# Optimization experiments

Measured on AMD Instinct MI355X. Metric: run time of the kernel, lower is better.

## Reference

```python
import jax, jax.numpy as jnp
import numpy as np

B, S, D = 4, 2048, 1024
H = 16
HD = D // H

def setup_inputs() -> dict:
    key = jax.random.key(0)
    ks = jax.random.split(key, 6)
    scale = 0.02
    return {
        "x": jax.random.normal(ks[0], (B, S, D), dtype=jnp.float32),
        "W_q": jax.random.normal(ks[1], (D, D), dtype=jnp.float32) * scale,
        "W_k": jax.random.normal(ks[2], (D, D), dtype=jnp.float32) * scale,
        "W_v": jax.random.normal(ks[3], (D, D), dtype=jnp.float32) * scale,
        "W_o": jax.random.normal(ks[4], (D, D), dtype=jnp.float32) * scale,
        "b_o": jax.random.normal(ks[5], (D,), dtype=jnp.float32) * scale,
    }

def reference(x, W_q, W_k, W_v, W_o, b_o):
    b, s, d = x.shape
    # projections, split heads: [b, h, s, hd]
    q = (x @ W_q).reshape(b, s, H, HD).transpose(0, 2, 1, 3)
    k = (x @ W_k).reshape(b, s, H, HD).transpose(0, 2, 1, 3)
    v = (x @ W_v).reshape(b, s, H, HD).transpose(0, 2, 1, 3)
    scores = jnp.einsum('bhqd,bhkd->bhqk', q, k)
    causal = jnp.triu(jnp.ones((s, s), dtype=bool), k=1)
    scores = jnp.where(causal, -jnp.inf, scores)
    # module divides by sqrt(hd) after masking; -inf stays -inf
    attn = jax.nn.softmax(scores / jnp.sqrt(jnp.float32(HD)), axis=-1)
    ctx = jnp.einsum('bhqk,bhkd->bhqd', attn, v)
    ctx = ctx.transpose(0, 2, 1, 3).reshape(b, s, d)
    return ctx @ W_o + b_o
```

## Files before the change

kernel.cpp:

```cpp
#include <hip/hip_runtime.h>
#include <hip/hip_bf16.h>
#include <math.h>

typedef __attribute__((ext_vector_type(8))) short bf16x8;
typedef __attribute__((ext_vector_type(4))) float f32x4;
typedef unsigned short u16;
typedef __hip_bfloat16 HB;

#define B_ 4
#define S_ 2048
#define D_ 1024
#define H_ 16
#define HD_ 64

__device__ __forceinline__ u16 f2b(float f) {
  HB h = __float2bfloat16(f);
  return *reinterpret_cast<u16*>(&h);
}
__device__ __forceinline__ void store1(HB* p, float v) { *p = __float2bfloat16(v); }
__device__ __forceinline__ void store1(float* p, float v) { *p = v; }

__device__ __forceinline__ float fexp2(float x) {
#if __has_builtin(__builtin_amdgcn_exp2f)
  return __builtin_amdgcn_exp2f(x);
#else
  return exp2f(x);
#endif
}

__device__ __forceinline__ void glds16(const u16* g, u16* l) {
  __builtin_amdgcn_global_load_lds(
      (const __attribute__((address_space(1))) void*)g,
      (__attribute__((address_space(3))) void*)l, 16, 0, 0);
}

__global__ __launch_bounds__(256) void cast_x(const float* __restrict__ xin,
                                              u16* __restrict__ xout) {
  const long i0 = ((long)blockIdx.x * 256 + threadIdx.x) * 8;
  bf16x8 r;
#pragma unroll
  for (int j = 0; j < 8; ++j) r[j] = (short)f2b(xin[i0 + j]);
  *(bf16x8*)(xout + i0) = r;
}

__global__ __launch_bounds__(256) void transpose_w(
    const float* __restrict__ w0, const float* __restrict__ w1,
    const float* __restrict__ w2, const float* __restrict__ w3,
    u16* __restrict__ out) {
  __shared__ __align__(16) u16 T[64 * 72];
  const float* Ws[4] = {w0, w1, w2, w3};
  const float* W = Ws[blockIdx.z];
  u16* Wt = out + (long)blockIdx.z * (1 << 20);
  const int t = threadIdx.x;
  const int r = t >> 3;
  const int c8 = (t & 7) * 8;
#pragma unroll
  for (int it = 0; it < 2; ++it) {
    const int row = blockIdx.y * 64 + it * 32 + r;
    const float* src = W + (long)row * D_ + blockIdx.x * 64 + c8;
#pragma unroll
    for (int j = 0; j < 8; ++j) T[(c8 + j) * 72 + it * 32 + r] = f2b(src[j]);
  }
  __syncthreads();
#pragma unroll
  for (int it = 0; it < 2; ++it) {
    const int row = it * 32 + r;
    bf16x8 v = *(const bf16x8*)(&T[row * 72 + c8]);
    *(bf16x8*)(Wt + (long)(blockIdx.x * 64 + row) * D_ + blockIdx.y * 64 + c8) = v;
  }
}

template <typename OT>
__global__ __launch_bounds__(256) void gemm_bt128(
    const u16* __restrict__ A, const u16* __restrict__ BTb, long bt_stride,
    OT* __restrict__ Cb, long c_stride, const float* __restrict__ bias,
    u16* __restrict__ vt, int scale_q, int M, int N, int K) {
  const u16* BT = BTb + (long)blockIdx.z * bt_stride;
  OT* C = Cb + (long)blockIdx.z * c_stride;

  __shared__ __align__(16) u16 As[128 * 32];
  __shared__ __align__(16) u16 Bs[128 * 32];

  const int tid = threadIdx.x;
  const int w = tid >> 6, lane = tid & 63;
  const int qr = lane & 15, quad = lane >> 4;
  const int wm = w >> 1, wn = w & 1;

  const long rowA0 = (long)blockIdx.y * 128;
  const long rowB0 = (long)blockIdx.x * 128;

  const int sr = lane >> 2;
  const int sc8 = ((lane & 3) ^ ((lane >> 3) & 3)) * 8;
  const long arow = rowA0 + w * 16 + sr;
  const long brow = rowB0 + w * 16 + sr;
  u16* asd0 = As + (w * 16) * 32;
  u16* asd1 = As + (64 + w * 16) * 32;
  u16* bsd0 = Bs + (w * 16) * 32;
  u16* bsd1 = Bs + (64 + w * 16) * 32;

  f32x4 acc[4][4] = {};

  for (int k0 = 0; k0 < K; k0 += 32) {
    __syncthreads();
    glds16(A + arow * K + k0 + sc8, asd0);
    glds16(A + (arow + 64) * K + k0 + sc8, asd1);
    glds16(BT + brow * K + k0 + sc8, bsd0);
    glds16(BT + (brow + 64) * K + k0 + sc8, bsd1);
    __syncthreads();

    bf16x8 af[4], bf[4];
#pragma unroll
    for (int ms = 0; ms < 4; ++ms) {
      const int m = wm * 64 + ms * 16 + qr;
      af[ms] = *(const bf16x8*)(&As[m * 32 + ((quad ^ ((m >> 1) & 3)) * 8)]);
    }
#pragma unroll
    for (int ns = 0; ns < 4; ++ns) {
      const int n = wn * 64 + ns * 16 + qr;
      bf[ns] = *(const bf16x8*)(&Bs[n * 32 + ((quad ^ ((n >> 1) & 3)) * 8)]);
    }

#pragma unroll
    for (int ms = 0; ms < 4; ++ms)
#pragma unroll
      for (int ns = 0; ns < 4; ++ns)
        acc[ms][ns] = __builtin_amdgcn_mfma_f32_16x16x32_bf16(
            af[ms], bf[ns], acc[ms][ns], 0, 0, 0);
  }

  if (vt && blockIdx.z == 2) {
#pragma unroll
    for (int ns = 0; ns < 4; ++ns) {
      const int col = (int)rowB0 + wn * 64 + ns * 16 + qr;
#pragma unroll
      for (int ms = 0; ms < 4; ++ms) {
        const long row = rowA0 + wm * 64 + ms * 16 + quad * 4;
        const long b = row >> 11, s = row & 2047;
        ushort4 pk;
        pk.x = f2b(acc[ms][ns][0]); pk.y = f2b(acc[ms][ns][1]);
        pk.z = f2b(acc[ms][ns][2]); pk.w = f2b(acc[ms][ns][3]);
        *(ushort4*)(vt + ((b * H_ + (col >> 6)) * HD_ + (col & 63)) * S_ + s) = pk;
      }
    }
    return;
  }

  const float qs = (scale_q && blockIdx.z == 0) ? 0.18033688011112042f : 1.f;
#pragma unroll
  for (int ns = 0; ns < 4; ++ns) {
    const long col = rowB0 + wn * 64 + ns * 16 + qr;
    const float bv = bias ? bias[col] : 0.f;
#pragma unroll
    for (int ms = 0; ms < 4; ++ms) {
      const long row = rowA0 + wm * 64 + ms * 16 + quad * 4;
#pragma unroll
      for (int r = 0; r < 4; ++r)
        store1(&C[(row + r) * (long)N + col], acc[ms][ns][r] * qs + bv);
    }
  }
}

__global__ __launch_bounds__(256) void attn5(
    const u16* __restrict__ Q, const u16* __restrict__ Kg,
    const u16* __restrict__ Vt, u16* __restrict__ ctx) {
  __shared__ __align__(16) u16 KV[2][2][64 * 64];
  __shared__ __align__(16) u16 Pl[4][16 * 64];

  const int tid = threadIdx.x;
  const int w = tid >> 6, lane = tid & 63;
  const int qr = lane & 15, quad = lane >> 4;
  const int bh = blockIdx.x;
  const int b = bh >> 4, h = bh & 15;

  const long baseQK = ((long)b * S_) * D_ + h * HD_;
  const long baseVt = (long)bh * HD_ * S_;

  const int sr8 = lane >> 3;
  const int sc8 = ((lane & 7) ^ sr8) * 8;

  const int tiles2[2] = {(int)blockIdx.y, 15 - (int)blockIdx.y};

#pragma unroll
  for (int ti = 0; ti < 2; ++ti) {
    const int q0 = tiles2[ti] * 128;
    const int qbase = q0 + w * 32;

    bf16x8 aq[2][2];
#pragma unroll
    for (int i = 0; i < 2; ++i) {
      const u16* qp_ = Q + baseQK + (long)(qbase + i * 16 + qr) * D_;
      aq[i][0] = *(const bf16x8*)(qp_ + quad * 8);
      aq[i][1] = *(const bf16x8*)(qp_ + 32 + quad * 8);
    }

    float li[2] = {};
    f32x4 o[2][4] = {};

    const int nkt = q0 / 64 + 2;

#pragma unroll
    for (int t = 0; t < 2; ++t) {
      const int r = t * 32 + w * 8 + sr8;
      glds16(Kg + baseQK + (long)r * D_ + sc8, &KV[0][0][(t * 32 + w * 8) * 64]);
      glds16(Vt + baseVt + (long)r * S_ + sc8, &KV[0][1][(t * 32 + w * 8) * 64]);
    }

    for (int kt = 0; kt < nkt; ++kt) {
      const int kbase = kt * 64;
      const int buf = kt & 1;

      __syncthreads();

      if (kt + 1 < nkt) {
        const int nb = kbase + 64;
#pragma unroll
        for (int t = 0; t < 2; ++t) {
          const int r = t * 32 + w * 8 + sr8;
          glds16(Kg + baseQK + (long)(nb + r) * D_ + sc8,
                 &KV[buf ^ 1][0][(t * 32 + w * 8) * 64]);
          glds16(Vt + baseVt + (long)r * S_ + nb + sc8,
                 &KV[buf ^ 1][1][(t * 32 + w * 8) * 64]);
        }
      }

      const u16* Ksb = KV[buf][0];
      const u16* Vsb = KV[buf][1];

      bf16x8 kf[4][2];
#pragma unroll
      for (int ns = 0; ns < 4; ++ns) {
        const int row = ns * 16 + qr;
        kf[ns][0] = *(const bf16x8*)(&Ksb[row * 64 + ((quad ^ (row & 7)) * 8)]);
        kf[ns][1] =
            *(const bf16x8*)(&Ksb[row * 64 + (((4 + quad) ^ (row & 7)) * 8)]);
      }

      f32x4 s[2][4] = {};
#pragma unroll
      for (int i = 0; i < 2; ++i)
#pragma unroll
        for (int ns = 0; ns < 4; ++ns) {
          s[i][ns] = __builtin_amdgcn_mfma_f32_16x16x32_bf16(
              kf[ns][0], aq[i][0], s[i][ns], 0, 0, 0);
          s[i][ns] = __builtin_amdgcn_mfma_f32_16x16x32_bf16(
              kf[ns][1], aq[i][1], s[i][ns], 0, 0, 0);
        }

#pragma unroll
      for (int i = 0; i < 2; ++i) {
        if (kbase + 64 > qbase + i * 16) {
          const int qrow = qbase + i * 16 + qr;
#pragma unroll
          for (int ns = 0; ns < 4; ++ns) {
            const int kc = kbase + ns * 16 + quad * 4;
#pragma unroll
            for (int r = 0; r < 4; ++r)
              if (kc + r > qrow) s[i][ns][r] = -1.0e30f;
          }
        }
      }

      bf16x8 vf[4][2];
#pragma unroll
      for (int ns = 0; ns < 4; ++ns) {
        const int row = ns * 16 + qr;
        vf[ns][0] = *(const bf16x8*)(&Vsb[row * 64 + ((quad ^ (row & 7)) * 8)]);
        vf[ns][1] =
            *(const bf16x8*)(&Vsb[row * 64 + (((4 + quad) ^ (row & 7)) * 8)]);
      }

#pragma unroll
      for (int i = 0; i < 2; ++i) {
        float ps = 0.f;
#pragma unroll
        for (int ns = 0; ns < 4; ++ns) {
          const float p0 = fexp2(s[i][ns][0]);
          const float p1 = fexp2(s[i][ns][1]);
          const float p2 = fexp2(s[i][ns][2]);
          const float p3 = fexp2(s[i][ns][3]);
          ps += (p0 + p1) + (p2 + p3);
          ushort4 pk;
          pk.x = f2b(p0); pk.y = f2b(p1); pk.z = f2b(p2); pk.w = f2b(p3);
          *(ushort4*)(&Pl[w][qr * 64 +
                             (((2 * ns + (quad >> 1)) ^ (qr & 7)) * 8) +
                             (quad & 1) * 4]) = pk;
        }
        ps += __shfl_xor(ps, 16, 64);
        ps += __shfl_xor(ps, 32, 64);
        li[i] += ps;

        bf16x8 pf0 = *(const bf16x8*)(&Pl[w][qr * 64 + ((quad ^ (qr & 7)) * 8)]);
        bf16x8 pf1 =
            *(const bf16x8*)(&Pl[w][qr * 64 + (((4 + quad) ^ (qr & 7)) * 8)]);
#pragma unroll
        for (int ns = 0; ns < 4; ++ns) {
          o[i][ns] = __builtin_amdgcn_mfma_f32_16x16x32_bf16(pf0, vf[ns][0],
                                                             o[i][ns], 0, 0, 0);
          o[i][ns] = __builtin_amdgcn_mfma_f32_16x16x32_bf16(pf1, vf[ns][1],
                                                             o[i][ns], 0, 0, 0);
        }
      }
    }

#pragma unroll
    for (int i = 0; i < 2; ++i)
#pragma unroll
      for (int r = 0; r < 4; ++r) {
        const float inv = 1.f / __shfl(li[i], quad * 4 + r, 64);
        const long row = qbase + i * 16 + quad * 4 + r;
#pragma unroll
        for (int ns = 0; ns < 4; ++ns)
          ctx[((long)b * S_ + row) * D_ + h * HD_ + ns * 16 + qr] =
              f2b(o[i][ns][r] * inv);
      }
  }
}

extern "C" void kernel_launch(void* const* d_in, const int* in_sizes, int n_in,
                              void* d_out, int out_size, void* d_ws,
                              size_t ws_size, hipStream_t stream) {
  const float* x  = (const float*)d_in[0];
  const float* Wq = (const float*)d_in[1];
  const float* Wk = (const float*)d_in[2];
  const float* Wv = (const float*)d_in[3];
  const float* Wo = (const float*)d_in[4];
  const float* bo = (const float*)d_in[5];

  u16* ws = (u16*)d_ws;
  u16* xb  = ws;
  u16* Wt  = xb + 8388608l;
  u16* Qb  = Wt + 4l * 1048576;
  u16* Kb  = Qb + 8388608l;
  u16* Vb  = Kb + 8388608l;
  u16* ctx = Qb;

  cast_x<<<4096, 256, 0, stream>>>(x, xb);

  transpose_w<<<dim3(16, 16, 4), 256, 0, stream>>>(Wq, Wk, Wv, Wo, Wt);

  gemm_bt128<HB><<<dim3(8, 64, 3), 256, 0, stream>>>(
      xb, Wt, 1048576l, (HB*)Qb, 8388608l, nullptr, Vb, 1, 8192, 1024, 1024);

  attn5<<<dim3(64, 8), 256, 0, stream>>>(Qb, Kb, Vb, ctx);

  gemm_bt128<float><<<dim3(8, 64, 1), 256, 0, stream>>>(
      ctx, Wt + 3l * 1048576, 0, (float*)d_out, 0, bo, nullptr, 0,
      8192, 1024, 1024);
}
```

Before: 282.8 us.

## Double-buffer GEMM K-tiles at 64 depth and remap blocks across XCDs

```diff
diff --git a/kernel.cpp b/kernel.cpp
--- a/kernel.cpp
+++ b/kernel.cpp
@@ -71,64 +71,80 @@
 }
 
 template <typename OT>
-__global__ __launch_bounds__(256) void gemm_bt128(
+__global__ __launch_bounds__(256) void gemm_bt128d(
     const u16* __restrict__ A, const u16* __restrict__ BTb, long bt_stride,
     OT* __restrict__ Cb, long c_stride, const float* __restrict__ bias,
     u16* __restrict__ vt, int scale_q, int M, int N, int K) {
-  const u16* BT = BTb + (long)blockIdx.z * bt_stride;
-  OT* C = Cb + (long)blockIdx.z * c_stride;
-
-  __shared__ __align__(16) u16 As[128 * 32];
-  __shared__ __align__(16) u16 Bs[128 * 32];
+  const int flat = ((int)blockIdx.z << 9) + ((int)blockIdx.y << 3) + blockIdx.x;
+  const int cpx = ((int)gridDim.z << 9) >> 3;
+  const int nf = (flat & 7) * cpx + (flat >> 3);
+  const int bz = nf >> 9;
+  const int rem = nf & 511;
+  const int by = rem >> 3, bx = rem & 7;
+
+  const u16* BT = BTb + (long)bz * bt_stride;
+  OT* C = Cb + (long)bz * c_stride;
+
+  __shared__ __align__(16) u16 As[2][128 * 64];
+  __shared__ __align__(16) u16 Bs[2][128 * 64];
 
   const int tid = threadIdx.x;
   const int w = tid >> 6, lane = tid & 63;
   const int qr = lane & 15, quad = lane >> 4;
   const int wm = w >> 1, wn = w & 1;
 
-  const long rowA0 = (long)blockIdx.y * 128;
-  const long rowB0 = (long)blockIdx.x * 128;
-
-  const int sr = lane >> 2;
-  const int sc8 = ((lane & 3) ^ ((lane >> 3) & 3)) * 8;
-  const long arow = rowA0 + w * 16 + sr;
-  const long brow = rowB0 + w * 16 + sr;
-  u16* asd0 = As + (w * 16) * 32;
-  u16* asd1 = As + (64 + w * 16) * 32;
-  u16* bsd0 = Bs + (w * 16) * 32;
-  u16* bsd1 = Bs + (64 + w * 16) * 32;
+  const long rowA0 = (long)by * 128;
+  const long rowB0 = (long)bx * 128;
+
+  const int sr8 = lane >> 3;
+  const int sc8 = ((lane & 7) ^ sr8) * 8;
 
   f32x4 acc[4][4] = {};
 
-  for (int k0 = 0; k0 < K; k0 += 32) {
+#define STAGE(nb, k0)                                                      \
+  {                                                                        \
+    _Pragma("unroll") for (int t = 0; t < 4; ++t) {                        \
+      const int r = w * 32 + t * 8;                                        \
+      glds16(A + (rowA0 + r + sr8) * K + (k0) + sc8, &As[nb][r * 64]);     \
+      glds16(BT + (rowB0 + r + sr8) * K + (k0) + sc8, &Bs[nb][r * 64]);    \
+    }                                                                      \
+  }
+
+  STAGE(0, 0);
+  __syncthreads();
+
+  const int NT = K >> 6;
+  for (int kt = 0; kt < NT; ++kt) {
+    const int b = kt & 1;
+    if (kt + 1 < NT) STAGE(b ^ 1, (kt + 1) << 6);
+
+#pragma unroll
+    for (int kk = 0; kk < 2; ++kk) {
+      bf16x8 af[4], bf[4];
+#pragma unroll
+      for (int ms = 0; ms < 4; ++ms) {
+        const int m = wm * 64 + ms * 16 + qr;
+        af[ms] = *(const bf16x8*)(&As[b][m * 64 +
+                                         (((kk * 4 + quad) ^ (m & 7)) * 8)]);
+      }
+#pragma unroll
+      for (int ns = 0; ns < 4; ++ns) {
+        const int n = wn * 64 + ns * 16 + qr;
+        bf[ns] = *(const bf16x8*)(&Bs[b][n * 64 +
+                                         (((kk * 4 + quad) ^ (n & 7)) * 8)]);
+      }
+#pragma unroll
+      for (int ms = 0; ms < 4; ++ms)
+#pragma unroll
+        for (int ns = 0; ns < 4; ++ns)
+          acc[ms][ns] = __builtin_amdgcn_mfma_f32_16x16x32_bf16(
+              af[ms], bf[ns], acc[ms][ns], 0, 0, 0);
+    }
     __syncthreads();
-    glds16(A + arow * K + k0 + sc8, asd0);
-    glds16(A + (arow + 64) * K + k0 + sc8, asd1);
-    glds16(BT + brow * K + k0 + sc8, bsd0);
-    glds16(BT + (brow + 64) * K + k0 + sc8, bsd1);
-    __syncthreads();
-
-    bf16x8 af[4], bf[4];
-#pragma unroll
-    for (int ms = 0; ms < 4; ++ms) {
-      const int m = wm * 64 + ms * 16 + qr;
-      af[ms] = *(const bf16x8*)(&As[m * 32 + ((quad ^ ((m >> 1) & 3)) * 8)]);
-    }
-#pragma unroll
-    for (int ns = 0; ns < 4; ++ns) {
-      const int n = wn * 64 + ns * 16 + qr;
-      bf[ns] = *(const bf16x8*)(&Bs[n * 32 + ((quad ^ ((n >> 1) & 3)) * 8)]);
-    }
-
-#pragma unroll
-    for (int ms = 0; ms < 4; ++ms)
-#pragma unroll
-      for (int ns = 0; ns < 4; ++ns)
-        acc[ms][ns] = __builtin_amdgcn_mfma_f32_16x16x32_bf16(
-            af[ms], bf[ns], acc[ms][ns], 0, 0, 0);
-  }
-
-  if (vt && blockIdx.z == 2) {
+  }
+#undef STAGE
+
+  if (vt && bz == 2) {
 #pragma unroll
     for (int ns = 0; ns < 4; ++ns) {
       const int col = (int)rowB0 + wn * 64 + ns * 16 + qr;
@@ -145,7 +161,7 @@
     return;
   }
 
-  const float qs = (scale_q && blockIdx.z == 0) ? 0.18033688011112042f : 1.f;
+  const float qs = (scale_q && bz == 0) ? 0.18033688011112042f : 1.f;
 #pragma unroll
   for (int ns = 0; ns < 4; ++ns) {
     const long col = rowB0 + wn * 64 + ns * 16 + qr;
@@ -338,12 +354,12 @@
 
   transpose_w<<<dim3(16, 16, 4), 256, 0, stream>>>(Wq, Wk, Wv, Wo, Wt);
 
-  gemm_bt128<HB><<<dim3(8, 64, 3), 256, 0, stream>>>(
+  gemm_bt128d<HB><<<dim3(8, 64, 3), 256, 0, stream>>>(
       xb, Wt, 1048576l, (HB*)Qb, 8388608l, nullptr, Vb, 1, 8192, 1024, 1024);
 
   attn5<<<dim3(64, 8), 256, 0, stream>>>(Qb, Kb, Vb, ctx);
 
-  gemm_bt128<float><<<dim3(8, 64, 1), 256, 0, stream>>>(
+  gemm_bt128d<float><<<dim3(8, 64, 1), 256, 0, stream>>>(
       ctx, Wt + 3l * 1048576, 0, (float*)d_out, 0, bo, nullptr, 0,
       8192, 1024, 1024);
 }
```

Measured after the change: 251.1 us. -11.2%, faster.
